# Optimization experiments

Hardware: AMD Instinct MI355X
Metric: run time of the kernel (lower is better)

Reference implementation:

```python
import jax, jax.numpy as jnp
import numpy as np

B, C, H, W = 8, 512, 32, 32
N = H * W
FG_THRES, BG_THRES, TOPK = 0.7, 0.6, 12


def setup_inputs() -> dict:
    key = jax.random.key(0)
    k1, k2, k3 = jax.random.split(key, 3)
    feature_q = jax.random.normal(k1, (B, C, H, W), dtype=jnp.float32)
    support_feat = jax.random.normal(k2, (B, C, H, W), dtype=jnp.float32)
    support_mask = jax.random.randint(k3, (B, H, W), 0, 2).astype(jnp.int32)
    return {"feature_q": feature_q, "support_feat": support_feat, "support_mask": support_mask}


def _masked_avg_pool(feat, mask):
    # feat [B,C,H,W], mask [B,1,H,W]; interpolate to same size is identity
    return jnp.sum(feat * mask, axis=(2, 3)) / (jnp.sum(mask, axis=(2, 3)) + 1e-5)


def _cosine(a, b):
    # F.cosine_similarity along channel dim 1 (eps=1e-8), with broadcasting
    dot = jnp.sum(a * b, axis=1)
    na = jnp.sqrt(jnp.sum(a * a, axis=1))
    nb = jnp.sqrt(jnp.sum(b * b, axis=1))
    return dot / jnp.maximum(na * nb, 1e-8)


def _similarity(feature_q, fg_proto, bg_proto):
    sim_fg = _cosine(feature_q, fg_proto)
    sim_bg = _cosine(feature_q, bg_proto)
    return jnp.stack([sim_bg, sim_fg], axis=1) * 10.0  # [B,2,H,W]


def _select_weights(pred, thres):
    # pred [N] -> float {0,1} selection weights; threshold mask, topk-12 fallback
    m = pred > thres
    _, top_idx = jax.lax.top_k(pred, TOPK)
    tm = jnp.zeros_like(m).at[top_idx].set(True)
    return jnp.where(m.sum() > 0, m, tm).astype(pred.dtype)


def _ssp_single(cur_feat, pred_fg, pred_bg):
    # cur_feat [C,N]; masked formulation == torch's variable-length column select
    wf = _select_weights(pred_fg, FG_THRES)
    wb = _select_weights(pred_bg, BG_THRES)
    fg_proto = jnp.sum(cur_feat * wf, axis=-1) / wf.sum()  # [C]
    bg_proto = jnp.sum(cur_feat * wb, axis=-1) / wb.sum()
    cn = cur_feat / jnp.sqrt(jnp.sum(cur_feat * cur_feat, axis=0, keepdims=True))
    sim = (cn.T @ cn) * 2.0  # [N,N] cosine sim, scaled
    neg = jnp.asarray(-1e30, sim.dtype)
    fg_attn = jax.nn.softmax(jnp.where(wf[None, :] > 0, sim, neg), axis=-1)
    bg_attn = jax.nn.softmax(jnp.where(wb[None, :] > 0, sim, neg), axis=-1)
    fg_local = (fg_attn @ cur_feat.T).T  # [C,N]
    bg_local = (bg_attn @ cur_feat.T).T
    return fg_proto, bg_proto, fg_local, bg_local


def reference(feature_q, support_feat, support_mask):
    mask_f = (support_mask == 1).astype(feature_q.dtype)[:, None]  # [B,1,H,W]
    mask_b = (support_mask == 0).astype(feature_q.dtype)[:, None]
    FP = _masked_avg_pool(support_feat, mask_f)[:, :, None, None]  # [B,C,1,1]
    BP = _masked_avg_pool(support_feat, mask_b)[:, :, None, None]
    out_0 = _similarity(feature_q, FP, BP)  # [B,2,H,W]
    pred = jax.nn.softmax(out_0, axis=1).reshape(B, 2, N)
    cur = feature_q.reshape(B, C, N)
    fg_p, bg_p, fg_l, bg_l = jax.vmap(_ssp_single)(cur, pred[:, 1], pred[:, 0])
    SSFP = fg_p[:, :, None, None]
    SSBP = bg_p[:, :, None, None]
    ASBP = bg_l.reshape(B, C, H, W)
    FP_1 = FP * 0.5 + SSFP * 0.5
    BP_1 = SSBP * 0.3 + ASBP * 0.7
    out_1 = _similarity(feature_q, FP_1, BP_1)  # [B,2,H,W]
    return out_1
```

## Files before the change

kernel.cpp:

```cpp
#include <hip/hip_runtime.h>
#include <math.h>

#define Bsz 8
#define Cch 512
#define Npx 1024
#define TOPK 12
#define BN (Bsz * Npx)

typedef __attribute__((ext_vector_type(8))) short bf16x8;
typedef __attribute__((ext_vector_type(4))) float f32x4;

__device__ __forceinline__ unsigned short f2bf(float x) {
    unsigned u = __float_as_uint(x);
    u += 0x7FFF + ((u >> 16) & 1);
    return (unsigned short)(u >> 16);
}
__device__ __forceinline__ float bf2f(unsigned short h) {
    return __uint_as_float(((unsigned)h) << 16);
}

__device__ __forceinline__ float warp_sum64(float v) {
    for (int o = 32; o > 0; o >>= 1) v += __shfl_down(v, o);
    return v;
}
__device__ __forceinline__ float block_sum256(float v, float* s4) {
    v = warp_sum64(v);
    int lane = threadIdx.x & 63, w = threadIdx.x >> 6;
    __syncthreads();
    if (lane == 0) s4[w] = v;
    __syncthreads();
    return s4[0] + s4[1] + s4[2] + s4[3];
}
__device__ __forceinline__ float block_sum512(float v, float* s8) {
    v = warp_sum64(v);
    int lane = threadIdx.x & 63, w = threadIdx.x >> 6;
    __syncthreads();
    if (lane == 0) s8[w] = v;
    __syncthreads();
    float r = 0.f;
    #pragma unroll
    for (int k = 0; k < 8; k++) r += s8[k];
    return r;
}

__global__ void k_pool(const float* __restrict__ sf, const int* __restrict__ mask,
                       float* __restrict__ FPo, float* __restrict__ BPo) {
    __shared__ float s4[4];
    int c = blockIdx.x, b = blockIdx.y, t = threadIdx.x;
    const float4* f4 = (const float4*)(sf + ((size_t)b * Cch + c) * Npx);
    const int4* m4 = (const int4*)(mask + (size_t)b * Npx);
    float4 v = f4[t];
    int4 m = m4[t];
    float sumf = (m.x == 1 ? v.x : 0.f) + (m.y == 1 ? v.y : 0.f)
               + (m.z == 1 ? v.z : 0.f) + (m.w == 1 ? v.w : 0.f);
    float tot = v.x + v.y + v.z + v.w;
    float cf = (float)((m.x == 1) + (m.y == 1) + (m.z == 1) + (m.w == 1));
    sumf = block_sum256(sumf, s4);
    tot  = block_sum256(tot, s4);
    cf   = block_sum256(cf, s4);
    if (t == 0) {
        FPo[b * Cch + c] = sumf / (cf + 1e-5f);
        BPo[b * Cch + c] = (tot - sumf) / ((1024.f - cf) + 1e-5f);
    }
}

__global__ void __launch_bounds__(512) k_predcast(const float* __restrict__ fq,
                       const float* __restrict__ FP, const float* __restrict__ BP,
                       float* __restrict__ dsim, float* __restrict__ invn,
                       unsigned short* __restrict__ Ft, float* __restrict__ accs) {
    __shared__ float sFP[Cch], sBP[Cch], s8[8];
    __shared__ float rdf[16][32], rdb[16][32], rqq[16][32];
    __shared__ unsigned short S[32][522];
    int b = blockIdx.y, t = threadIdx.x;
    int tx = t & 31, ty = t >> 5;
    int p0 = blockIdx.x * 32;
    int p = p0 + tx;
    if (t < 160) accs[(size_t)(t >> 5) * BN + b * Npx + p0 + (t & 31)] = 0.f;
    sFP[t] = FP[b * Cch + t];
    sBP[t] = BP[b * Cch + t];
    __syncthreads();
    float nf = sqrtf(block_sum512(sFP[t] * sFP[t], s8));
    float nb = sqrtf(block_sum512(sBP[t] * sBP[t], s8));
    const float* q = fq + (size_t)b * Cch * Npx + p;
    float df = 0.f, db = 0.f, qq = 0.f;
    int c0 = ty * 32;
    #pragma unroll 4
    for (int c = 0; c < 32; c += 2) {
        float v0 = q[(size_t)(c0 + c) * Npx];
        float v1 = q[(size_t)(c0 + c + 1) * Npx];
        df += v0 * sFP[c0 + c] + v1 * sFP[c0 + c + 1];
        db += v0 * sBP[c0 + c] + v1 * sBP[c0 + c + 1];
        qq += v0 * v0 + v1 * v1;
        unsigned pk = (unsigned)f2bf(v0) | ((unsigned)f2bf(v1) << 16);
        *(unsigned*)&S[tx][c0 + c] = pk;
    }
    rdf[ty][tx] = df; rdb[ty][tx] = db; rqq[ty][tx] = qq;
    __syncthreads();
    for (int s = 8; s > 0; s >>= 1) {
        if (ty < s) {
            rdf[ty][tx] += rdf[ty + s][tx];
            rdb[ty][tx] += rdb[ty + s][tx];
            rqq[ty][tx] += rqq[ty + s][tx];
        }
        __syncthreads();
    }
    if (ty == 0) {
        float nq = sqrtf(rqq[0][tx]);
        float simf = 10.f * rdf[0][tx] / fmaxf(nq * nf, 1e-8f);
        float simb = 10.f * rdb[0][tx] / fmaxf(nq * nb, 1e-8f);
        dsim[b * Npx + p] = simf - simb;
        invn[b * Npx + p] = 1.f / nq;
    }
    int w = t >> 6, lane = t & 63;
    unsigned short* FtB = Ft + (size_t)b * Npx * Cch;
    for (int pr = w; pr < 32; pr += 8) {
        unsigned* dst = (unsigned*)(FtB + (size_t)(p0 + pr) * Cch);
        #pragma unroll
        for (int it = 0; it < 4; it++) {
            int d = it * 64 + lane;
            dst[d] = *(const unsigned*)&S[pr][d * 2];
        }
    }
}

__global__ void __launch_bounds__(1024) k_selcompact(const float* __restrict__ dsim,
                        const float* __restrict__ invn,
                        const unsigned short* __restrict__ Ft,
                        const float* __restrict__ FP,
                        int* __restrict__ nsf, int* __restrict__ nsb,
                        int* __restrict__ jf, int* __restrict__ jb,
                        float* __restrict__ ivg,
                        float* __restrict__ fgp, float* __restrict__ bgp,
                        float* __restrict__ FP1, float* __restrict__ nfv) {
    __shared__ int wsum[16];
    __shared__ int sns;
    __shared__ float sProto[16][512];
    __shared__ float s16f[16];
    int b = blockIdx.y, t = threadIdx.x;
    int lane = t & 63, w = t >> 6;
    bool isf = (blockIdx.x == 0);
    float d = dsim[b * Npx + t];
    float key = isf ? d : -d;
    float thres = isf ? 0.8472979f : 0.4054651f;
    int flag = (key > thres) ? 1 : 0;
    int x = flag;
    #pragma unroll
    for (int o = 1; o < 64; o <<= 1) {
        int y = __shfl_up(x, o);
        if (lane >= o) x += y;
    }
    if (lane == 63) wsum[w] = x;
    __syncthreads();
    int base = 0, total = 0;
    #pragma unroll
    for (int k = 0; k < 16; k++) {
        int s = wsum[k];
        if (k < w) base += s;
        total += s;
    }
    int* jdst = (isf ? jf : jb) + b * Npx;
    if (total == 0) {
        __shared__ int   sc[Npx];
        __shared__ float v[Npx];
        __shared__ float rv[Npx];
        __shared__ int   ri[Npx];
        v[t] = key; flag = 0;
        __syncthreads();
        for (int k = 0; k < TOPK; k++) {
            rv[t] = v[t]; ri[t] = t;
            __syncthreads();
            for (int s = 512; s > 0; s >>= 1) {
                if (t < s) {
                    float a = rv[t], bb = rv[t + s];
                    int ia = ri[t], ib = ri[t + s];
                    if (bb > a || (bb == a && ib < ia)) { rv[t] = bb; ri[t] = ib; }
                }
                __syncthreads();
            }
            int win = ri[0];
            if (t == win) { flag = 1; v[t] = -INFINITY; }
            __syncthreads();
        }
        sc[t] = flag;
        __syncthreads();
        for (int off = 1; off < 1024; off <<= 1) {
            int xx = (t >= off) ? sc[t - off] : 0;
            __syncthreads();
            sc[t] += xx;
            __syncthreads();
        }
        if (flag) {
            int pos = sc[t] - 1;
            jdst[pos] = t;
            if (!isf) ivg[b * Npx + pos] = invn[b * Npx + t];
        }
        if (t == 1023) sns = sc[1023];
    } else {
        if (flag) {
            int pos = base + x - 1;
            jdst[pos] = t;
            if (!isf) ivg[b * Npx + pos] = invn[b * Npx + t];
        }
        if (t == 0) sns = total;
    }
    __syncthreads();
    int ns = sns;
    if (t == 0) (isf ? nsf : nsb)[b] = ns;
    const unsigned short* FtB = Ft + (size_t)b * Npx * Cch;
    float facc[8] = {0.f, 0.f, 0.f, 0.f, 0.f, 0.f, 0.f, 0.f};
    int k = w;
    int row = (k < ns) ? jdst[k] : 0;
    while (k < ns) {
        int kn = k + 16;
        int rown = (kn < ns) ? jdst[kn] : 0;
        bf16x8 vv = *(const bf16x8*)&FtB[(size_t)row * Cch + lane * 8];
        #pragma unroll
        for (int e = 0; e < 8; e++) facc[e] += bf2f((unsigned short)vv[e]);
        k = kn; row = rown;
    }
    #pragma unroll
    for (int e = 0; e < 8; e++) sProto[w][lane * 8 + e] = facc[e];
    __syncthreads();
    float fp1 = 0.f;
    if (t < 512) {
        float s = 0.f;
        #pragma unroll
        for (int q = 0; q < 16; q++) s += sProto[q][t];
        float pv = s / (float)ns;
        (isf ? fgp : bgp)[b * Cch + t] = pv;
        if (isf) {
            fp1 = 0.5f * FP[b * Cch + t] + 0.5f * pv;
            FP1[b * Cch + t] = fp1;
        }
    }
    if (isf) {
        float v2 = warp_sum64(fp1 * fp1);
        if (lane == 0) s16f[w] = v2;
        __syncthreads();
        if (t == 0) {
            float nn = 0.f;
            #pragma unroll
            for (int q = 0; q < 16; q++) nn += s16f[q];
            nfv[b] = sqrtf(nn);
        }
    }
}

__global__ void __launch_bounds__(256) k_gram_fused(const unsigned short* __restrict__ Ft,
                        const int* __restrict__ jb, const int* __restrict__ nsb,
                        const float* __restrict__ invn, const float* __restrict__ ivg,
                        unsigned short* __restrict__ G, unsigned short* __restrict__ Fg,
                        float* __restrict__ denom) {
    int b = blockIdx.z;
    int ns = nsb[b];
    int KC = (ns + 31) & ~31;
    if (blockIdx.y >= 16) {
        int j0 = blockIdx.x * 64;
        if (j0 >= KC) return;
        int c0 = (blockIdx.y - 16) * 32;
        __shared__ unsigned short tt[64][34];
        const unsigned short* S = Ft + (size_t)b * Npx * Cch;
        const int* ji = jb + b * Npx;
        int col = threadIdx.x & 31, rr = threadIdx.x >> 5;
        for (int r = rr; r < 64; r += 8) {
            int j = j0 + r;
            int src = (j < ns) ? ji[j] : ji[0];
            tt[r][col] = S[(size_t)src * Cch + c0 + col];
        }
        __syncthreads();
        unsigned* D32 = (unsigned*)(Fg + (size_t)b * Cch * Npx);
        int jx = threadIdx.x & 31;
        for (int cr = rr; cr < 32; cr += 8) {
            unsigned lo = tt[2 * jx][cr], hi = tt[2 * jx + 1][cr];
            D32[(size_t)(c0 + cr) * (Npx / 2) + (j0 >> 1) + jx] = lo | (hi << 16);
        }
        return;
    }
    int j0 = blockIdx.y * 64;
    if (j0 >= KC) return;
    int i0 = blockIdx.x * 64;
    __shared__ unsigned short At[64][72];
    __shared__ unsigned short Bt[64][72];
    __shared__ int sji[64];
    __shared__ float sfi[64], sfj[64];
    const unsigned short* FA = Ft + (size_t)b * Npx * Cch;
    int tid = threadIdx.x;
    if (tid < 64) {
        int j = j0 + tid;
        sji[tid] = (j < ns) ? jb[b * Npx + j] : jb[b * Npx];
        sfj[tid] = (j < ns) ? ivg[b * Npx + j] : 0.f;
        sfi[tid] = 2.f * invn[b * Npx + i0 + tid];
    }
    __syncthreads();
    int rA = tid >> 2, kc8 = (tid & 3) * 8;
    const unsigned short* sa = FA + (size_t)(i0 + rA) * Cch + kc8;
    const unsigned short* sb = FA + (size_t)sji[rA] * Cch + kc8;
    int l = tid & 63, w = tid >> 6;
    int ml = l & 15, quad = l >> 4;
    f32x4 acc[4] = {};
    uint4 a0 = *(const uint4*)sa,        a1 = *(const uint4*)(sa + 32);
    uint4 b0 = *(const uint4*)sb,        b1 = *(const uint4*)(sb + 32);
    for (int k0 = 0; k0 < Cch; k0 += 64) {
        __syncthreads();
        *(uint4*)&At[rA][kc8] = a0;  *(uint4*)&At[rA][kc8 + 32] = a1;
        *(uint4*)&Bt[rA][kc8] = b0;  *(uint4*)&Bt[rA][kc8 + 32] = b1;
        __syncthreads();
        int kn = k0 + 64;
        if (kn < Cch) {
            a0 = *(const uint4*)(sa + kn);  a1 = *(const uint4*)(sa + kn + 32);
            b0 = *(const uint4*)(sb + kn);  b1 = *(const uint4*)(sb + kn + 32);
        }
        #pragma unroll
        for (int h = 0; h < 2; h++) {
            bf16x8 af = *(const bf16x8*)&At[w * 16 + ml][quad * 8 + h * 32];
            bf16x8 bfr[4];
            #pragma unroll
            for (int v = 0; v < 4; v++) bfr[v] = *(const bf16x8*)&Bt[v * 16 + ml][quad * 8 + h * 32];
            #pragma unroll
            for (int v = 0; v < 4; v++)
                acc[v] = __builtin_amdgcn_mfma_f32_16x16x32_bf16(af, bfr[v], acc[v], 0, 0, 0);
        }
    }
    unsigned short* g = G + (size_t)b * Npx * Npx;
    float* dn = denom + b * Npx;
    #pragma unroll
    for (int r = 0; r < 4; r++) {
        int il = w * 16 + quad * 4 + r;
        float fi = sfi[il];
        float s = 0.f;
        #pragma unroll
        for (int v = 0; v < 4; v++) {
            int jl = v * 16 + ml;
            float e = 0.f;
            if (j0 + jl < ns) e = __expf(acc[v][r] * fi * sfj[jl]);
            unsigned short eb = f2bf(e);
            g[(size_t)(i0 + il) * Npx + j0 + jl] = eb;
            s += bf2f(eb);
        }
        #pragma unroll
        for (int m = 1; m < 16; m <<= 1) s += __shfl_xor(s, m);
        if (ml == 0) atomicAdd(&dn[i0 + il], s);
    }
}

__global__ void __launch_bounds__(256) k_pv_c(const unsigned short* __restrict__ Fg,
                                              const unsigned short* __restrict__ A,
                                              const unsigned short* __restrict__ Ft,
                                              const int* __restrict__ nsb,
                                              const float* __restrict__ denom,
                                              const float* __restrict__ bgp,
                                              const float* __restrict__ FP1,
                                              float* __restrict__ accs) {
    int b = blockIdx.z;
    int KC64 = ((((nsb[b] + 31) & ~31) + 63) & ~63);
    __shared__ unsigned short At[64][72];
    __shared__ unsigned short Bt[64][72];
    __shared__ float sfp1[64], sbg[64];
    __shared__ float spdb[64], spnb[64], spdf[64], spqq[64];
    int i0 = blockIdx.x * 64, c0 = blockIdx.y * 64;
    const unsigned short* F = Fg + (size_t)b * Cch * Npx;
    const unsigned short* Ar = A + (size_t)b * Npx * Npx;
    int tid = threadIdx.x;
    if (tid < 64) {
        sfp1[tid] = FP1[b * Cch + c0 + tid];
        sbg[tid] = 0.3f * bgp[b * Cch + c0 + tid];
    }
    int rr = tid >> 2, kc8 = (tid & 3) * 8;
    const unsigned short* sa = F + (size_t)(c0 + rr) * Npx + kc8;
    const unsigned short* sb = Ar + (size_t)(i0 + rr) * Npx + kc8;
    int l = tid & 63, w = tid >> 6;
    int ml = l & 15, quad = l >> 4;
    f32x4 acc[4] = {};
    uint4 a0 = *(const uint4*)sa,  a1 = *(const uint4*)(sa + 32);
    uint4 b0 = *(const uint4*)sb,  b1 = *(const uint4*)(sb + 32);
    for (int j0 = 0; j0 < KC64; j0 += 64) {
        __syncthreads();
        *(uint4*)&At[rr][kc8] = a0;  *(uint4*)&At[rr][kc8 + 32] = a1;
        *(uint4*)&Bt[rr][kc8] = b0;  *(uint4*)&Bt[rr][kc8 + 32] = b1;
        __syncthreads();
        int jn = j0 + 64;
        if (jn < KC64) {
            a0 = *(const uint4*)(sa + jn);  a1 = *(const uint4*)(sa + jn + 32);
            b0 = *(const uint4*)(sb + jn);  b1 = *(const uint4*)(sb + jn + 32);
        }
        #pragma unroll
        for (int h = 0; h < 2; h++) {
            bf16x8 af = *(const bf16x8*)&At[w * 16 + ml][quad * 8 + h * 32];
            bf16x8 bfr[4];
            #pragma unroll
            for (int v = 0; v < 4; v++) bfr[v] = *(const bf16x8*)&Bt[v * 16 + ml][quad * 8 + h * 32];
            #pragma unroll
            for (int v = 0; v < 4; v++)
                acc[v] = __builtin_amdgcn_mfma_f32_16x16x32_bf16(af, bfr[v], acc[v], 0, 0, 0);
        }
    }
    __syncthreads();
    {
        const unsigned short* src = Ft + (size_t)b * Npx * Cch + (size_t)(i0 + (tid >> 2)) * Cch + c0 + (tid & 3) * 16;
        *(uint4*)&At[tid >> 2][(tid & 3) * 16] = *(const uint4*)src;
        *(uint4*)&At[tid >> 2][(tid & 3) * 16 + 8] = *(const uint4*)(src + 8);
    }
    if (tid < 64) { spdb[tid] = 0.f; spnb[tid] = 0.f; spdf[tid] = 0.f; spqq[tid] = 0.f; }
    float rd[4];
    #pragma unroll
    for (int v = 0; v < 4; v++) rd[v] = 1.f / denom[b * Npx + i0 + v * 16 + ml];
    __syncthreads();
    #pragma unroll
    for (int v = 0; v < 4; v++) {
        int iloc = v * 16 + ml;
        float sdb = 0.f, snb = 0.f, sdf = 0.f, sqq = 0.f;
        #pragma unroll
        for (int r = 0; r < 4; r++) {
            int cl = w * 16 + quad * 4 + r;
            float loc = acc[v][r] * rd[v];
            float bp1 = sbg[cl] + 0.7f * loc;
            float qv = bf2f(At[iloc][cl]);
            sdb += qv * bp1;
            snb += bp1 * bp1;
            sdf += qv * sfp1[cl];
            sqq += qv * qv;
        }
        #pragma unroll
        for (int m = 16; m < 64; m <<= 1) {
            sdb += __shfl_xor(sdb, m);
            snb += __shfl_xor(snb, m);
            sdf += __shfl_xor(sdf, m);
            sqq += __shfl_xor(sqq, m);
        }
        if (quad == 0) {
            atomicAdd(&spdb[iloc], sdb);
            atomicAdd(&spnb[iloc], snb);
            atomicAdd(&spdf[iloc], sdf);
            atomicAdd(&spqq[iloc], sqq);
        }
    }
    __syncthreads();
    if (tid < 256) {
        int a = tid >> 6, idx = tid & 63;
        float v = (a == 0) ? spdb[idx] : (a == 1) ? spnb[idx] : (a == 2) ? spdf[idx] : spqq[idx];
        atomicAdd(&accs[(size_t)(a + 1) * BN + b * Npx + i0 + idx], v);
    }
}

__global__ void k_fin(const float* __restrict__ accs, const float* __restrict__ nfv,
                      float* __restrict__ out) {
    int b = blockIdx.y;
    int p = blockIdx.x * 256 + threadIdx.x;
    int base = b * Npx + p;
    float db = accs[(size_t)1 * BN + base];
    float nb = accs[(size_t)2 * BN + base];
    float df = accs[(size_t)3 * BN + base];
    float qq = accs[(size_t)4 * BN + base];
    float nq = sqrtf(qq);
    float sf = 10.f * df / fmaxf(nq * nfv[b], 1e-8f);
    float sb = 10.f * db / fmaxf(nq * sqrtf(nb), 1e-8f);
    out[((size_t)b * 2) * Npx + p] = sb;
    out[((size_t)b * 2 + 1) * Npx + p] = sf;
}

extern "C" void kernel_launch(void* const* d_in, const int* in_sizes, int n_in,
                              void* d_out, int out_size, void* d_ws, size_t ws_size,
                              hipStream_t stream) {
    const float* fq = (const float*)d_in[0];
    const float* sf = (const float*)d_in[1];
    const int* mask = (const int*)d_in[2];
    float* out = (float*)d_out;

    float* ws = (float*)d_ws;
    float* FP    = ws;
    float* BP    = FP + Bsz * Cch;
    float* fgp   = BP + Bsz * Cch;
    float* bgp   = fgp + Bsz * Cch;
    float* FP1   = bgp + Bsz * Cch;
    float* nfv   = FP1 + Bsz * Cch;
    float* dsim  = nfv + 8;
    float* invn  = dsim + BN;
    float* ivg   = invn + BN;
    int*   nsf   = (int*)(ivg + BN);
    int*   nsb   = nsf + 8;
    int*   jf    = nsb + 8;
    int*   jb    = jf + BN;
    float* accs  = (float*)(jb + BN);
    unsigned short* Ft = (unsigned short*)(accs + (size_t)5 * BN);
    unsigned short* Fg = Ft + (size_t)Bsz * Npx * Cch;
    unsigned short* Gb = Fg + (size_t)Bsz * Cch * Npx;

    float* denom = accs;

    k_pool<<<dim3(Cch, Bsz), 256, 0, stream>>>(sf, mask, FP, BP);
    k_predcast<<<dim3(Npx / 32, Bsz), 512, 0, stream>>>(fq, FP, BP, dsim, invn, Ft, accs);
    k_selcompact<<<dim3(2, Bsz), 1024, 0, stream>>>(dsim, invn, Ft, FP, nsf, nsb, jf, jb, ivg, fgp, bgp, FP1, nfv);
    k_gram_fused<<<dim3(16, 32, Bsz), 256, 0, stream>>>(Ft, jb, nsb, invn, ivg, Gb, Fg, denom);
    k_pv_c<<<dim3(Npx / 64, Cch / 64, Bsz), 256, 0, stream>>>(Fg, Gb, Ft, nsb, denom, bgp, FP1, accs);
    k_fin<<<dim3(Npx / 256, Bsz), 256, 0, stream>>>(accs, nfv, out);
}
```

Measured before the change: 134.1 us.

## Fuse finalize into PV kernel, recompute softmax denominators, merge pool reductions

The softmax denominator is no longer built with atomics in the gram kernel. The PV kernel now sums the bf16 probability tiles it already loads, which removes one accumulator buffer and the atomic traffic. The separate finalize kernel is folded into the PV kernel through a per-batch completion counter, so the last block writes the outputs and one launch is saved. k_pool merges its three block reductions so they share one barrier; in exchange, the last-block pattern adds a serial tail and relies on threadfence ordering.

```diff
diff --git a/kernel.cpp b/kernel.cpp
--- a/kernel.cpp
+++ b/kernel.cpp
@@ -23,14 +23,6 @@
     for (int o = 32; o > 0; o >>= 1) v += __shfl_down(v, o);
     return v;
 }
-__device__ __forceinline__ float block_sum256(float v, float* s4) {
-    v = warp_sum64(v);
-    int lane = threadIdx.x & 63, w = threadIdx.x >> 6;
-    __syncthreads();
-    if (lane == 0) s4[w] = v;
-    __syncthreads();
-    return s4[0] + s4[1] + s4[2] + s4[3];
-}
 __device__ __forceinline__ float block_sum512(float v, float* s8) {
     v = warp_sum64(v);
     int lane = threadIdx.x & 63, w = threadIdx.x >> 6;
@@ -45,7 +37,7 @@
 
 __global__ void k_pool(const float* __restrict__ sf, const int* __restrict__ mask,
                        float* __restrict__ FPo, float* __restrict__ BPo) {
-    __shared__ float s4[4];
+    __shared__ float s4a[4], s4b[4], s4c[4];
     int c = blockIdx.x, b = blockIdx.y, t = threadIdx.x;
     const float4* f4 = (const float4*)(sf + ((size_t)b * Cch + c) * Npx);
     const int4* m4 = (const int4*)(mask + (size_t)b * Npx);
@@ -55,19 +47,26 @@
                + (m.z == 1 ? v.z : 0.f) + (m.w == 1 ? v.w : 0.f);
     float tot = v.x + v.y + v.z + v.w;
     float cf = (float)((m.x == 1) + (m.y == 1) + (m.z == 1) + (m.w == 1));
-    sumf = block_sum256(sumf, s4);
-    tot  = block_sum256(tot, s4);
-    cf   = block_sum256(cf, s4);
+    sumf = warp_sum64(sumf);
+    tot  = warp_sum64(tot);
+    cf   = warp_sum64(cf);
+    int lane = t & 63, w = t >> 6;
+    if (lane == 0) { s4a[w] = sumf; s4b[w] = tot; s4c[w] = cf; }
+    __syncthreads();
     if (t == 0) {
-        FPo[b * Cch + c] = sumf / (cf + 1e-5f);
-        BPo[b * Cch + c] = (tot - sumf) / ((1024.f - cf) + 1e-5f);
+        float sA = s4a[0] + s4a[1] + s4a[2] + s4a[3];
+        float sB = s4b[0] + s4b[1] + s4b[2] + s4b[3];
+        float sC = s4c[0] + s4c[1] + s4c[2] + s4c[3];
+        FPo[b * Cch + c] = sA / (sC + 1e-5f);
+        BPo[b * Cch + c] = (sB - sA) / ((1024.f - sC) + 1e-5f);
     }
 }
 
 __global__ void __launch_bounds__(512) k_predcast(const float* __restrict__ fq,
                        const float* __restrict__ FP, const float* __restrict__ BP,
                        float* __restrict__ dsim, float* __restrict__ invn,
-                       unsigned short* __restrict__ Ft, float* __restrict__ accs) {
+                       unsigned short* __restrict__ Ft, float* __restrict__ accs,
+                       int* __restrict__ wcnt) {
     __shared__ float sFP[Cch], sBP[Cch], s8[8];
     __shared__ float rdf[16][32], rdb[16][32], rqq[16][32];
     __shared__ unsigned short S[32][522];
@@ -75,7 +74,8 @@
     int tx = t & 31, ty = t >> 5;
     int p0 = blockIdx.x * 32;
     int p = p0 + tx;
-    if (t < 160) accs[(size_t)(t >> 5) * BN + b * Npx + p0 + (t & 31)] = 0.f;
+    if (t < 128) accs[(size_t)(t >> 5) * BN + b * Npx + p0 + (t & 31)] = 0.f;
+    if (blockIdx.x == 0 && t == 0) wcnt[b] = 0;
     sFP[t] = FP[b * Cch + t];
     sBP[t] = BP[b * Cch + t];
     __syncthreads();
@@ -249,8 +249,7 @@
 __global__ void __launch_bounds__(256) k_gram_fused(const unsigned short* __restrict__ Ft,
                         const int* __restrict__ jb, const int* __restrict__ nsb,
                         const float* __restrict__ invn, const float* __restrict__ ivg,
-                        unsigned short* __restrict__ G, unsigned short* __restrict__ Fg,
-                        float* __restrict__ denom) {
+                        unsigned short* __restrict__ G, unsigned short* __restrict__ Fg) {
     int b = blockIdx.z;
     int ns = nsb[b];
     int KC = (ns + 31) & ~31;
@@ -322,24 +321,17 @@
         }
     }
     unsigned short* g = G + (size_t)b * Npx * Npx;
-    float* dn = denom + b * Npx;
     #pragma unroll
     for (int r = 0; r < 4; r++) {
         int il = w * 16 + quad * 4 + r;
         float fi = sfi[il];
-        float s = 0.f;
         #pragma unroll
         for (int v = 0; v < 4; v++) {
             int jl = v * 16 + ml;
             float e = 0.f;
             if (j0 + jl < ns) e = __expf(acc[v][r] * fi * sfj[jl]);
-            unsigned short eb = f2bf(e);
-            g[(size_t)(i0 + il) * Npx + j0 + jl] = eb;
-            s += bf2f(eb);
-        }
-        #pragma unroll
-        for (int m = 1; m < 16; m <<= 1) s += __shfl_xor(s, m);
-        if (ml == 0) atomicAdd(&dn[i0 + il], s);
+            g[(size_t)(i0 + il) * Npx + j0 + jl] = f2bf(e);
+        }
     }
 }
 
@@ -347,15 +339,17 @@
                                               const unsigned short* __restrict__ A,
                                               const unsigned short* __restrict__ Ft,
                                               const int* __restrict__ nsb,
-                                              const float* __restrict__ denom,
                                               const float* __restrict__ bgp,
                                               const float* __restrict__ FP1,
-                                              float* __restrict__ accs) {
+                                              float* __restrict__ accs,
+                                              const float* __restrict__ nfv,
+                                              int* __restrict__ wcnt,
+                                              float* __restrict__ out) {
     int b = blockIdx.z;
     int KC64 = ((((nsb[b] + 31) & ~31) + 63) & ~63);
     __shared__ unsigned short At[64][72];
     __shared__ unsigned short Bt[64][72];
-    __shared__ float sfp1[64], sbg[64];
+    __shared__ float sfp1[64], sbg[64], sden[64];
     __shared__ float spdb[64], spnb[64], spdf[64], spqq[64];
     int i0 = blockIdx.x * 64, c0 = blockIdx.y * 64;
     const unsigned short* F = Fg + (size_t)b * Cch * Npx;
@@ -371,12 +365,21 @@
     int l = tid & 63, w = tid >> 6;
     int ml = l & 15, quad = l >> 4;
     f32x4 acc[4] = {};
+    float dsum = 0.f;
     uint4 a0 = *(const uint4*)sa,  a1 = *(const uint4*)(sa + 32);
     uint4 b0 = *(const uint4*)sb,  b1 = *(const uint4*)(sb + 32);
     for (int j0 = 0; j0 < KC64; j0 += 64) {
         __syncthreads();
         *(uint4*)&At[rr][kc8] = a0;  *(uint4*)&At[rr][kc8 + 32] = a1;
         *(uint4*)&Bt[rr][kc8] = b0;  *(uint4*)&Bt[rr][kc8 + 32] = b1;
+        dsum += __uint_as_float(b0.x << 16) + __uint_as_float(b0.x & 0xFFFF0000u)
+              + __uint_as_float(b0.y << 16) + __uint_as_float(b0.y & 0xFFFF0000u)
+              + __uint_as_float(b0.z << 16) + __uint_as_float(b0.z & 0xFFFF0000u)
+              + __uint_as_float(b0.w << 16) + __uint_as_float(b0.w & 0xFFFF0000u)
+              + __uint_as_float(b1.x << 16) + __uint_as_float(b1.x & 0xFFFF0000u)
+              + __uint_as_float(b1.y << 16) + __uint_as_float(b1.y & 0xFFFF0000u)
+              + __uint_as_float(b1.z << 16) + __uint_as_float(b1.z & 0xFFFF0000u)
+              + __uint_as_float(b1.w << 16) + __uint_as_float(b1.w & 0xFFFF0000u);
         __syncthreads();
         int jn = j0 + 64;
         if (jn < KC64) {
@@ -394,6 +397,9 @@
                 acc[v] = __builtin_amdgcn_mfma_f32_16x16x32_bf16(af, bfr[v], acc[v], 0, 0, 0);
         }
     }
+    dsum += __shfl_xor(dsum, 1);
+    dsum += __shfl_xor(dsum, 2);
+    if ((tid & 3) == 0) sden[rr] = dsum;
     __syncthreads();
     {
         const unsigned short* src = Ft + (size_t)b * Npx * Cch + (size_t)(i0 + (tid >> 2)) * Cch + c0 + (tid & 3) * 16;
@@ -403,7 +409,7 @@
     if (tid < 64) { spdb[tid] = 0.f; spnb[tid] = 0.f; spdf[tid] = 0.f; spqq[tid] = 0.f; }
     float rd[4];
     #pragma unroll
-    for (int v = 0; v < 4; v++) rd[v] = 1.f / denom[b * Npx + i0 + v * 16 + ml];
+    for (int v = 0; v < 4; v++) rd[v] = 1.f / sden[v * 16 + ml];
     __syncthreads();
     #pragma unroll
     for (int v = 0; v < 4; v++) {
@@ -435,27 +441,32 @@
         }
     }
     __syncthreads();
-    if (tid < 256) {
+    {
         int a = tid >> 6, idx = tid & 63;
         float v = (a == 0) ? spdb[idx] : (a == 1) ? spnb[idx] : (a == 2) ? spdf[idx] : spqq[idx];
-        atomicAdd(&accs[(size_t)(a + 1) * BN + b * Npx + i0 + idx], v);
-    }
-}
-
-__global__ void k_fin(const float* __restrict__ accs, const float* __restrict__ nfv,
-                      float* __restrict__ out) {
-    int b = blockIdx.y;
-    int p = blockIdx.x * 256 + threadIdx.x;
-    int base = b * Npx + p;
-    float db = accs[(size_t)1 * BN + base];
-    float nb = accs[(size_t)2 * BN + base];
-    float df = accs[(size_t)3 * BN + base];
-    float qq = accs[(size_t)4 * BN + base];
-    float nq = sqrtf(qq);
-    float sf = 10.f * df / fmaxf(nq * nfv[b], 1e-8f);
-    float sb = 10.f * db / fmaxf(nq * sqrtf(nb), 1e-8f);
-    out[((size_t)b * 2) * Npx + p] = sb;
-    out[((size_t)b * 2 + 1) * Npx + p] = sf;
+        atomicAdd(&accs[(size_t)a * BN + b * Npx + i0 + idx], v);
+    }
+    __syncthreads();
+    __threadfence();
+    __shared__ int lastF;
+    if (tid == 0) lastF = (atomicAdd(&wcnt[b], 1) == (16 * 8 - 1)) ? 1 : 0;
+    __syncthreads();
+    if (lastF) {
+        __threadfence();
+        float nfb = nfv[b];
+        for (int q = tid; q < Npx; q += 256) {
+            int base = b * Npx + q;
+            float db = accs[(size_t)0 * BN + base];
+            float nb = accs[(size_t)1 * BN + base];
+            float df = accs[(size_t)2 * BN + base];
+            float qq = accs[(size_t)3 * BN + base];
+            float nq = sqrtf(qq);
+            float sf = 10.f * df / fmaxf(nq * nfb, 1e-8f);
+            float sb2 = 10.f * db / fmaxf(nq * sqrtf(nb), 1e-8f);
+            out[((size_t)b * 2) * Npx + q] = sb2;
+            out[((size_t)b * 2 + 1) * Npx + q] = sf;
+        }
+    }
 }
 
 extern "C" void kernel_launch(void* const* d_in, const int* in_sizes, int n_in,
@@ -481,16 +492,14 @@
     int*   jf    = nsb + 8;
     int*   jb    = jf + BN;
     float* accs  = (float*)(jb + BN);
-    unsigned short* Ft = (unsigned short*)(accs + (size_t)5 * BN);
+    int*   wcnt  = (int*)(accs + (size_t)4 * BN);
+    unsigned short* Ft = (unsigned short*)(wcnt + 8);
     unsigned short* Fg = Ft + (size_t)Bsz * Npx * Cch;
     unsigned short* Gb = Fg + (size_t)Bsz * Cch * Npx;
 
-    float* denom = accs;
-
     k_pool<<<dim3(Cch, Bsz), 256, 0, stream>>>(sf, mask, FP, BP);
-    k_predcast<<<dim3(Npx / 32, Bsz), 512, 0, stream>>>(fq, FP, BP, dsim, invn, Ft, accs);
+    k_predcast<<<dim3(Npx / 32, Bsz), 512, 0, stream>>>(fq, FP, BP, dsim, invn, Ft, accs, wcnt);
     k_selcompact<<<dim3(2, Bsz), 1024, 0, stream>>>(dsim, invn, Ft, FP, nsf, nsb, jf, jb, ivg, fgp, bgp, FP1, nfv);
-    k_gram_fused<<<dim3(16, 32, Bsz), 256, 0, stream>>>(Ft, jb, nsb, invn, ivg, Gb, Fg, denom);
-    k_pv_c<<<dim3(Npx / 64, Cch / 64, Bsz), 256, 0, stream>>>(Fg, Gb, Ft, nsb, denom, bgp, FP1, accs);
-    k_fin<<<dim3(Npx / 256, Bsz), 256, 0, stream>>>(accs, nfv, out);
-}
+    k_gram_fused<<<dim3(16, 32, Bsz), 256, 0, stream>>>(Ft, jb, nsb, invn, ivg, Gb, Fg);
+    k_pv_c<<<dim3(Npx / 64, Cch / 64, Bsz), 256, 0, stream>>>(Fg, Gb, Ft, nsb, bgp, FP1, accs, nfv, wcnt, out);
+}
```

Result: slower. 198.9 us (+48.3%).
